# Optimization experiments

Measured on AMD Instinct MI355X. Metric: run time of the kernel, lower is better.

Reference implementation:

```python
import jax, jax.numpy as jnp
import numpy as np
from jax import lax

# Dims fixed by the module: Linear(96,24) => 16 channels * (24/4) length => per-step feature L=24
L = 24

def _conv1d(x, w, b):
    # x: (N, Cin, L), w: (Cout, Cin, K), 'same' padding for K=3
    y = lax.conv_general_dilated(x, w, window_strides=(1,), padding=[(1, 1)],
                                 dimension_numbers=("NCH", "OIH", "NCH"))
    return y + b[None, :, None]

def _maxpool2(x):
    # x: (N, C, L) -> (N, C, L//2), non-overlapping window of 2
    n, c, l = x.shape
    return x.reshape(n, c, l // 2, 2).max(axis=-1)

def setup_inputs() -> dict:
    key = jax.random.key(0)
    ks = jax.random.split(key, 11)
    S, B = 512, 256
    def u(k, shape, fan_in):
        bound = 1.0 / np.sqrt(fan_in)
        return jax.random.uniform(k, shape, jnp.float32, -bound, bound)
    return {
        "x":   jax.random.normal(ks[0], (S, B, L), jnp.float32),
        "w11": u(ks[1], (8, 1, 3), 1 * 3),   "b11": u(ks[2], (8,), 1 * 3),
        "w12": u(ks[3], (8, 8, 3), 8 * 3),   "b12": u(ks[4], (8,), 8 * 3),
        "w21": u(ks[5], (16, 8, 3), 8 * 3),  "b21": u(ks[6], (16,), 8 * 3),
        "w22": u(ks[7], (16, 16, 3), 16 * 3), "b22": u(ks[8], (16,), 16 * 3),
        "Wl":  u(ks[9], (24, 96), 96),        "bl": u(ks[10], (24,), 96),
    }

def reference(x, w11, b11, w12, b12, w21, b21, w22, b22, Wl, bl):
    # Original loops over timesteps applying the same CNN; timestep and batch
    # are independent, so fuse them into one conv batch (identical math).
    S, B, Lf = x.shape
    h = x.reshape(S * B, 1, Lf)                 # (SB, 1, 24)
    h = jax.nn.relu(_conv1d(h, w11, b11))       # (SB, 8, 24); Dropout(0.1) = identity in eval
    h = jax.nn.relu(_conv1d(h, w12, b12))       # (SB, 8, 24)
    h = _maxpool2(h)                            # (SB, 8, 12)
    h = jax.nn.relu(_conv1d(h, w21, b21))       # (SB, 16, 12); Dropout = identity in eval
    h = jax.nn.relu(_conv1d(h, w22, b22))       # (SB, 16, 12)
    h = _maxpool2(h)                            # (SB, 16, 6)
    h = h.reshape(S, B, 96)                     # torch reshape(batch, -1) per step
    return h @ Wl.T + bl                        # (S, B, 24)
```

## Files before the change

kernel.cpp:

```cpp
#include <hip/hip_runtime.h>


typedef _Float16 h2v __attribute__((ext_vector_type(2)));

__device__ __forceinline__ float fdot2(h2v a, h2v b, float c) {
    return __builtin_amdgcn_fdot2(a, b, c, false);
}
__device__ __forceinline__ unsigned packh2(float a, float b) {
    h2v p; p.x = (_Float16)a; p.y = (_Float16)b;
    return __builtin_bit_cast(unsigned, p);
}
__device__ __forceinline__ h2v ldh2(unsigned u) {
    return __builtin_bit_cast(h2v, u);
}

#define TPB 256

__launch_bounds__(TPB, 3)
__global__ void cnn_pre_lstm_kernel(
    const float* __restrict__ x,
    const float* __restrict__ w11, const float* __restrict__ b11,
    const float* __restrict__ w12, const float* __restrict__ b12,
    const float* __restrict__ w21, const float* __restrict__ b21,
    const float* __restrict__ w22, const float* __restrict__ b22,
    const float* __restrict__ Wl,  const float* __restrict__ bl,
    float* __restrict__ out)
{
    __shared__ unsigned sA_[6144];
    __shared__ unsigned sB_[3072];
    float* sInF  = (float*)sB_;
    float* sOutF = (float*)sA_;

    const int tid = threadIdx.x;
    const int ln  = tid & 63;
    const int wv  = __builtin_amdgcn_readfirstlane(tid >> 6);

    {
        const float* xg = x + (size_t)blockIdx.x * 1536;
        #pragma unroll
        for (int k = 0; k < 6; ++k) {
            int o = tid + k * TPB;
            int s = o / 24, p = o % 24;
            sInF[s * 25 + p] = xg[o];
        }
    }
    __syncthreads();

    {
        const int c0 = 2 * wv;
        const float wA0 = w11[c0*3+0], wA1 = w11[c0*3+1], wA2 = w11[c0*3+2];
        const float wB0 = w11[c0*3+3], wB1 = w11[c0*3+4], wB2 = w11[c0*3+5];
        const float bA = b11[c0], bB = b11[c0+1];

        float xv[24];
        #pragma unroll
        for (int p = 0; p < 24; ++p) xv[p] = sInF[ln*25 + p];

        #pragma unroll
        for (int p = 0; p < 24; ++p) {
            float a = bA, b = bB;
            if (p > 0)  { a = fmaf(wA0, xv[p-1], a); b = fmaf(wB0, xv[p-1], b); }
            a = fmaf(wA1, xv[p], a);  b = fmaf(wB1, xv[p], b);
            if (p < 23) { a = fmaf(wA2, xv[p+1], a); b = fmaf(wB2, xv[p+1], b); }
            sA_[wv*1536 + p*64 + ln] = packh2(fmaxf(a, 0.f), fmaxf(b, 0.f));
        }
    }
    __syncthreads();

    {
        const int c0 = 2 * wv;
        h2v wp[2][4][3];
        #pragma unroll
        for (int i = 0; i < 2; ++i)
            #pragma unroll
            for (int cp = 0; cp < 4; ++cp)
                #pragma unroll
                for (int k = 0; k < 3; ++k) {
                    const float* wr = w12 + (c0 + i) * 24;
                    wp[i][cp][k] = ldh2(packh2(wr[(2*cp)*3 + k], wr[(2*cp+1)*3 + k]));
                }
        float acc[2][24];
        {
            const float bb0 = b12[c0], bb1 = b12[c0+1];
            #pragma unroll
            for (int p = 0; p < 24; ++p) { acc[0][p] = bb0; acc[1][p] = bb1; }
        }
        #pragma unroll
        for (int cp = 0; cp < 4; ++cp) {
            h2v xv[24];
            #pragma unroll
            for (int p = 0; p < 24; ++p) xv[p] = ldh2(sA_[cp*1536 + p*64 + ln]);
            #pragma unroll
            for (int p = 0; p < 24; ++p) {
                #pragma unroll
                for (int i = 0; i < 2; ++i) {
                    if (p > 0)  acc[i][p] = fdot2(wp[i][cp][0], xv[p-1], acc[i][p]);
                    acc[i][p] = fdot2(wp[i][cp][1], xv[p], acc[i][p]);
                    if (p < 23) acc[i][p] = fdot2(wp[i][cp][2], xv[p+1], acc[i][p]);
                }
            }
        }
        #pragma unroll
        for (int q = 0; q < 12; ++q) {
            float r0 = fmaxf(fmaxf(acc[0][2*q], acc[0][2*q+1]), 0.f);
            float r1 = fmaxf(fmaxf(acc[1][2*q], acc[1][2*q+1]), 0.f);
            sB_[wv*768 + q*64 + ln] = packh2(r0, r1);
        }
    }
    __syncthreads();

    {
        const int c0 = 4 * wv;
        h2v wp[4][4][3];
        #pragma unroll
        for (int i = 0; i < 4; ++i)
            #pragma unroll
            for (int cp = 0; cp < 4; ++cp)
                #pragma unroll
                for (int k = 0; k < 3; ++k) {
                    const float* wr = w21 + (c0 + i) * 24;
                    wp[i][cp][k] = ldh2(packh2(wr[(2*cp)*3 + k], wr[(2*cp+1)*3 + k]));
                }
        float acc[4][12];
        #pragma unroll
        for (int i = 0; i < 4; ++i) {
            const float bb = b21[c0 + i];
            #pragma unroll
            for (int p = 0; p < 12; ++p) acc[i][p] = bb;
        }
        #pragma unroll
        for (int cp = 0; cp < 4; ++cp) {
            h2v xv[12];
            #pragma unroll
            for (int p = 0; p < 12; ++p) xv[p] = ldh2(sB_[cp*768 + p*64 + ln]);
            #pragma unroll
            for (int p = 0; p < 12; ++p) {
                #pragma unroll
                for (int i = 0; i < 4; ++i) {
                    if (p > 0)  acc[i][p] = fdot2(wp[i][cp][0], xv[p-1], acc[i][p]);
                    acc[i][p] = fdot2(wp[i][cp][1], xv[p], acc[i][p]);
                    if (p < 11) acc[i][p] = fdot2(wp[i][cp][2], xv[p+1], acc[i][p]);
                }
            }
        }
        #pragma unroll
        for (int pr = 0; pr < 2; ++pr)
            #pragma unroll
            for (int p = 0; p < 12; ++p)
                sA_[(2*wv + pr)*768 + p*64 + ln] =
                    packh2(fmaxf(acc[2*pr][p], 0.f), fmaxf(acc[2*pr+1][p], 0.f));
    }
    __syncthreads();

    {
        const int c0 = 4 * wv;
        float acc[4][12];
        #pragma unroll
        for (int i = 0; i < 4; ++i) {
            const float bb = b22[c0 + i];
            #pragma unroll
            for (int p = 0; p < 12; ++p) acc[i][p] = bb;
        }
        #pragma unroll
        for (int hh = 0; hh < 2; ++hh) {
            h2v wp[4][4][3];
            #pragma unroll
            for (int i = 0; i < 4; ++i)
                #pragma unroll
                for (int cp = 0; cp < 4; ++cp)
                    #pragma unroll
                    for (int k = 0; k < 3; ++k) {
                        const float* wr = w22 + (c0 + i) * 48;
                        const int ci0 = 2 * (4*hh + cp);
                        wp[i][cp][k] = ldh2(packh2(wr[ci0*3 + k], wr[(ci0+1)*3 + k]));
                    }
            #pragma unroll
            for (int cp = 0; cp < 4; ++cp) {
                const int gcp = 4*hh + cp;
                h2v xv[12];
                #pragma unroll
                for (int p = 0; p < 12; ++p) xv[p] = ldh2(sA_[gcp*768 + p*64 + ln]);
                #pragma unroll
                for (int p = 0; p < 12; ++p) {
                    #pragma unroll
                    for (int i = 0; i < 4; ++i) {
                        if (p > 0)  acc[i][p] = fdot2(wp[i][cp][0], xv[p-1], acc[i][p]);
                        acc[i][p] = fdot2(wp[i][cp][1], xv[p], acc[i][p]);
                        if (p < 11) acc[i][p] = fdot2(wp[i][cp][2], xv[p+1], acc[i][p]);
                    }
                }
            }
        }
        #pragma unroll
        for (int pr = 0; pr < 2; ++pr)
            #pragma unroll
            for (int q = 0; q < 6; ++q) {
                float r0 = fmaxf(fmaxf(acc[2*pr][2*q],   acc[2*pr][2*q+1]),   0.f);
                float r1 = fmaxf(fmaxf(acc[2*pr+1][2*q], acc[2*pr+1][2*q+1]), 0.f);
                sB_[(2*wv + pr)*384 + q*64 + ln] = packh2(r0, r1);
            }
    }
    __syncthreads();

    {
        const int j0 = 6 * wv;
        float v[96];
        #pragma unroll
        for (int cp = 0; cp < 8; ++cp)
            #pragma unroll
            for (int q = 0; q < 6; ++q) {
                h2v t = ldh2(sB_[cp*384 + q*64 + ln]);
                v[12*cp + q]     = (float)t.x;
                v[12*cp + q + 6] = (float)t.y;
            }
        float acc6[6];
        #pragma unroll
        for (int i = 0; i < 6; ++i) acc6[i] = bl[j0 + i];
        #pragma unroll
        for (int i = 0; i < 6; ++i) {
            const float4* wr = (const float4*)(Wl + (j0 + i) * 96);
            #pragma unroll
            for (int g = 0; g < 24; ++g) {
                float4 w4 = wr[g];
                acc6[i] = fmaf(w4.x, v[4*g+0], fmaf(w4.y, v[4*g+1],
                          fmaf(w4.z, v[4*g+2], fmaf(w4.w, v[4*g+3], acc6[i]))));
            }
        }
        #pragma unroll
        for (int i = 0; i < 6; ++i)
            sOutF[ln*25 + j0 + i] = acc6[i];
    }
    __syncthreads();

    {
        float* og = out + (size_t)blockIdx.x * 1536;
        #pragma unroll
        for (int k = 0; k < 6; ++k) {
            int o = tid + k * TPB;
            int s = o / 24, j = o % 24;
            og[o] = sOutF[s*25 + j];
        }
    }
}

extern "C" void kernel_launch(void* const* d_in, const int* in_sizes, int n_in,
                              void* d_out, int out_size, void* d_ws, size_t ws_size,
                              hipStream_t stream) {
    const float* x   = (const float*)d_in[0];
    const float* w11 = (const float*)d_in[1];
    const float* b11 = (const float*)d_in[2];
    const float* w12 = (const float*)d_in[3];
    const float* b12 = (const float*)d_in[4];
    const float* w21 = (const float*)d_in[5];
    const float* b21 = (const float*)d_in[6];
    const float* w22 = (const float*)d_in[7];
    const float* b22 = (const float*)d_in[8];
    const float* Wl  = (const float*)d_in[9];
    const float* bl  = (const float*)d_in[10];
    float* out = (float*)d_out;

    const int n_samples = in_sizes[0] / 24;
    const int blocks = n_samples / 64;

    hipLaunchKernelGGL(cnn_pre_lstm_kernel, dim3(blocks), dim3(TPB), 0, stream,
                       x, w11, b11, w12, b12, w21, b21, w22, b22, Wl, bl, out);
}
```

Measured before the change: 138.8 us.

## Prepack fp16 weights in a separate kernel, use fdot2 for linear, double block size

A small pre-kernel packs the conv and linear weights into fp16 pairs in workspace once per call, so the main kernel loads packed words instead of converting floats in every thread. The final linear layer now uses fp16 fdot2 on the packed activations and weights instead of fp32 FMAs. Blocks grow to 512 threads covering 128 samples, with twice the shared memory. The trade-offs are an extra kernel launch, lower precision in the linear layer, and possibly lower occupancy from the larger LDS footprint.

```diff
diff --git a/kernel.cpp b/kernel.cpp
--- a/kernel.cpp
+++ b/kernel.cpp
@@ -14,29 +14,60 @@
     return __builtin_bit_cast(h2v, u);
 }
 
-#define TPB 256
-
-__launch_bounds__(TPB, 3)
+#define W12P 0
+#define W21P 96
+#define W22P 288
+#define WLP  672
+#define NPACK 1824
+
+__global__ void pack_weights_kernel(
+    const float* __restrict__ w12, const float* __restrict__ w21,
+    const float* __restrict__ w22, const float* __restrict__ Wl,
+    unsigned* __restrict__ ws)
+{
+    for (int i = threadIdx.x; i < NPACK; i += 256) {
+        float a, b;
+        if (i < W21P) {
+            int t = i - W12P, co = t / 12, r = t % 12, cp = r / 3, k = r % 3;
+            a = w12[co*24 + (2*cp)*3 + k];  b = w12[co*24 + (2*cp+1)*3 + k];
+        } else if (i < W22P) {
+            int t = i - W21P, co = t / 12, r = t % 12, cp = r / 3, k = r % 3;
+            a = w21[co*24 + (2*cp)*3 + k];  b = w21[co*24 + (2*cp+1)*3 + k];
+        } else if (i < WLP) {
+            int t = i - W22P, co = t / 24, r = t % 24, cp = r / 3, k = r % 3;
+            a = w22[co*48 + (2*cp)*3 + k];  b = w22[co*48 + (2*cp+1)*3 + k];
+        } else {
+            int t = i - WLP, j = t / 48, r = t % 48, cp = r / 6, q = r % 6;
+            a = Wl[j*96 + 12*cp + q];       b = Wl[j*96 + 12*cp + q + 6];
+        }
+        ws[i] = packh2(a, b);
+    }
+}
+
+#define TPB 512
+
+__launch_bounds__(TPB, 4)
 __global__ void cnn_pre_lstm_kernel(
     const float* __restrict__ x,
     const float* __restrict__ w11, const float* __restrict__ b11,
-    const float* __restrict__ w12, const float* __restrict__ b12,
-    const float* __restrict__ w21, const float* __restrict__ b21,
-    const float* __restrict__ w22, const float* __restrict__ b22,
-    const float* __restrict__ Wl,  const float* __restrict__ bl,
+    const float* __restrict__ b12, const float* __restrict__ b21,
+    const float* __restrict__ b22, const float* __restrict__ bl,
+    const unsigned* __restrict__ wsp,
     float* __restrict__ out)
 {
-    __shared__ unsigned sA_[6144];
-    __shared__ unsigned sB_[3072];
+    __shared__ unsigned sA_[12288];
+    __shared__ unsigned sB_[6144];
     float* sInF  = (float*)sB_;
     float* sOutF = (float*)sA_;
 
     const int tid = threadIdx.x;
     const int ln  = tid & 63;
     const int wv  = __builtin_amdgcn_readfirstlane(tid >> 6);
-
-    {
-        const float* xg = x + (size_t)blockIdx.x * 1536;
+    const int cg  = wv & 3;
+    const int ls  = (wv >> 2) * 64 + ln;
+
+    {
+        const float* xg = x + (size_t)blockIdx.x * 3072;
         #pragma unroll
         for (int k = 0; k < 6; ++k) {
             int o = tid + k * TPB;
@@ -47,14 +78,14 @@
     __syncthreads();
 
     {
-        const int c0 = 2 * wv;
+        const int c0 = 2 * cg;
         const float wA0 = w11[c0*3+0], wA1 = w11[c0*3+1], wA2 = w11[c0*3+2];
         const float wB0 = w11[c0*3+3], wB1 = w11[c0*3+4], wB2 = w11[c0*3+5];
         const float bA = b11[c0], bB = b11[c0+1];
 
         float xv[24];
         #pragma unroll
-        for (int p = 0; p < 24; ++p) xv[p] = sInF[ln*25 + p];
+        for (int p = 0; p < 24; ++p) xv[p] = sInF[ls*25 + p];
 
         #pragma unroll
         for (int p = 0; p < 24; ++p) {
@@ -62,23 +93,21 @@
             if (p > 0)  { a = fmaf(wA0, xv[p-1], a); b = fmaf(wB0, xv[p-1], b); }
             a = fmaf(wA1, xv[p], a);  b = fmaf(wB1, xv[p], b);
             if (p < 23) { a = fmaf(wA2, xv[p+1], a); b = fmaf(wB2, xv[p+1], b); }
-            sA_[wv*1536 + p*64 + ln] = packh2(fmaxf(a, 0.f), fmaxf(b, 0.f));
-        }
-    }
-    __syncthreads();
-
-    {
-        const int c0 = 2 * wv;
+            sA_[cg*3072 + p*128 + ls] = packh2(fmaxf(a, 0.f), fmaxf(b, 0.f));
+        }
+    }
+    __syncthreads();
+
+    {
+        const int c0 = 2 * cg;
         h2v wp[2][4][3];
         #pragma unroll
         for (int i = 0; i < 2; ++i)
             #pragma unroll
             for (int cp = 0; cp < 4; ++cp)
                 #pragma unroll
-                for (int k = 0; k < 3; ++k) {
-                    const float* wr = w12 + (c0 + i) * 24;
-                    wp[i][cp][k] = ldh2(packh2(wr[(2*cp)*3 + k], wr[(2*cp+1)*3 + k]));
-                }
+                for (int k = 0; k < 3; ++k)
+                    wp[i][cp][k] = ldh2(wsp[W12P + (c0+i)*12 + cp*3 + k]);
         float acc[2][24];
         {
             const float bb0 = b12[c0], bb1 = b12[c0+1];
@@ -89,7 +118,7 @@
         for (int cp = 0; cp < 4; ++cp) {
             h2v xv[24];
             #pragma unroll
-            for (int p = 0; p < 24; ++p) xv[p] = ldh2(sA_[cp*1536 + p*64 + ln]);
+            for (int p = 0; p < 24; ++p) xv[p] = ldh2(sA_[cp*3072 + p*128 + ls]);
             #pragma unroll
             for (int p = 0; p < 24; ++p) {
                 #pragma unroll
@@ -104,23 +133,21 @@
         for (int q = 0; q < 12; ++q) {
             float r0 = fmaxf(fmaxf(acc[0][2*q], acc[0][2*q+1]), 0.f);
             float r1 = fmaxf(fmaxf(acc[1][2*q], acc[1][2*q+1]), 0.f);
-            sB_[wv*768 + q*64 + ln] = packh2(r0, r1);
-        }
-    }
-    __syncthreads();
-
-    {
-        const int c0 = 4 * wv;
+            sB_[cg*1536 + q*128 + ls] = packh2(r0, r1);
+        }
+    }
+    __syncthreads();
+
+    {
+        const int c0 = 4 * cg;
         h2v wp[4][4][3];
         #pragma unroll
         for (int i = 0; i < 4; ++i)
             #pragma unroll
             for (int cp = 0; cp < 4; ++cp)
                 #pragma unroll
-                for (int k = 0; k < 3; ++k) {
-                    const float* wr = w21 + (c0 + i) * 24;
-                    wp[i][cp][k] = ldh2(packh2(wr[(2*cp)*3 + k], wr[(2*cp+1)*3 + k]));
-                }
+                for (int k = 0; k < 3; ++k)
+                    wp[i][cp][k] = ldh2(wsp[W21P + (c0+i)*12 + cp*3 + k]);
         float acc[4][12];
         #pragma unroll
         for (int i = 0; i < 4; ++i) {
@@ -132,7 +159,7 @@
         for (int cp = 0; cp < 4; ++cp) {
             h2v xv[12];
             #pragma unroll
-            for (int p = 0; p < 12; ++p) xv[p] = ldh2(sB_[cp*768 + p*64 + ln]);
+            for (int p = 0; p < 12; ++p) xv[p] = ldh2(sB_[cp*1536 + p*128 + ls]);
             #pragma unroll
             for (int p = 0; p < 12; ++p) {
                 #pragma unroll
@@ -147,13 +174,13 @@
         for (int pr = 0; pr < 2; ++pr)
             #pragma unroll
             for (int p = 0; p < 12; ++p)
-                sA_[(2*wv + pr)*768 + p*64 + ln] =
+                sA_[(2*cg + pr)*1536 + p*128 + ls] =
                     packh2(fmaxf(acc[2*pr][p], 0.f), fmaxf(acc[2*pr+1][p], 0.f));
     }
     __syncthreads();
 
     {
-        const int c0 = 4 * wv;
+        const int c0 = 4 * cg;
         float acc[4][12];
         #pragma unroll
         for (int i = 0; i < 4; ++i) {
@@ -169,17 +196,14 @@
                 #pragma unroll
                 for (int cp = 0; cp < 4; ++cp)
                     #pragma unroll
-                    for (int k = 0; k < 3; ++k) {
-                        const float* wr = w22 + (c0 + i) * 48;
-                        const int ci0 = 2 * (4*hh + cp);
-                        wp[i][cp][k] = ldh2(packh2(wr[ci0*3 + k], wr[(ci0+1)*3 + k]));
-                    }
+                    for (int k = 0; k < 3; ++k)
+                        wp[i][cp][k] = ldh2(wsp[W22P + (c0+i)*24 + (4*hh+cp)*3 + k]);
             #pragma unroll
             for (int cp = 0; cp < 4; ++cp) {
                 const int gcp = 4*hh + cp;
                 h2v xv[12];
                 #pragma unroll
-                for (int p = 0; p < 12; ++p) xv[p] = ldh2(sA_[gcp*768 + p*64 + ln]);
+                for (int p = 0; p < 12; ++p) xv[p] = ldh2(sA_[gcp*1536 + p*128 + ls]);
                 #pragma unroll
                 for (int p = 0; p < 12; ++p) {
                     #pragma unroll
@@ -197,43 +221,43 @@
             for (int q = 0; q < 6; ++q) {
                 float r0 = fmaxf(fmaxf(acc[2*pr][2*q],   acc[2*pr][2*q+1]),   0.f);
                 float r1 = fmaxf(fmaxf(acc[2*pr+1][2*q], acc[2*pr+1][2*q+1]), 0.f);
-                sB_[(2*wv + pr)*384 + q*64 + ln] = packh2(r0, r1);
-            }
-    }
-    __syncthreads();
-
-    {
-        const int j0 = 6 * wv;
-        float v[96];
+                sB_[(2*cg + pr)*768 + q*128 + ls] = packh2(r0, r1);
+            }
+    }
+    __syncthreads();
+
+    {
+        const int j0 = 6 * cg;
+        h2v hv[8][6];
         #pragma unroll
         for (int cp = 0; cp < 8; ++cp)
             #pragma unroll
-            for (int q = 0; q < 6; ++q) {
-                h2v t = ldh2(sB_[cp*384 + q*64 + ln]);
-                v[12*cp + q]     = (float)t.x;
-                v[12*cp + q + 6] = (float)t.y;
-            }
+            for (int q = 0; q < 6; ++q)
+                hv[cp][q] = ldh2(sB_[cp*768 + q*128 + ls]);
+
         float acc6[6];
         #pragma unroll
         for (int i = 0; i < 6; ++i) acc6[i] = bl[j0 + i];
         #pragma unroll
         for (int i = 0; i < 6; ++i) {
-            const float4* wr = (const float4*)(Wl + (j0 + i) * 96);
-            #pragma unroll
-            for (int g = 0; g < 24; ++g) {
-                float4 w4 = wr[g];
-                acc6[i] = fmaf(w4.x, v[4*g+0], fmaf(w4.y, v[4*g+1],
-                          fmaf(w4.z, v[4*g+2], fmaf(w4.w, v[4*g+3], acc6[i]))));
+            #pragma unroll
+            for (int cp = 0; cp < 8; ++cp) {
+                #pragma unroll
+                for (int qq = 0; qq < 3; ++qq) {
+                    uint2 w2 = *(const uint2*)&wsp[WLP + (j0+i)*48 + cp*6 + 2*qq];
+                    acc6[i] = fdot2(ldh2(w2.x), hv[cp][2*qq],   acc6[i]);
+                    acc6[i] = fdot2(ldh2(w2.y), hv[cp][2*qq+1], acc6[i]);
+                }
             }
         }
         #pragma unroll
         for (int i = 0; i < 6; ++i)
-            sOutF[ln*25 + j0 + i] = acc6[i];
-    }
-    __syncthreads();
-
-    {
-        float* og = out + (size_t)blockIdx.x * 1536;
+            sOutF[ls*25 + j0 + i] = acc6[i];
+    }
+    __syncthreads();
+
+    {
+        float* og = out + (size_t)blockIdx.x * 3072;
         #pragma unroll
         for (int k = 0; k < 6; ++k) {
             int o = tid + k * TPB;
@@ -258,10 +282,14 @@
     const float* Wl  = (const float*)d_in[9];
     const float* bl  = (const float*)d_in[10];
     float* out = (float*)d_out;
+    unsigned* ws = (unsigned*)d_ws;
+
+    hipLaunchKernelGGL(pack_weights_kernel, dim3(1), dim3(256), 0, stream,
+                       w12, w21, w22, Wl, ws);
 
     const int n_samples = in_sizes[0] / 24;
-    const int blocks = n_samples / 64;
+    const int blocks = n_samples / 128;
 
     hipLaunchKernelGGL(cnn_pre_lstm_kernel, dim3(blocks), dim3(TPB), 0, stream,
-                       x, w11, b11, w12, b12, w21, b21, w22, b22, Wl, bl, out);
-}
+                       x, w11, b11, b12, b21, b22, bl, ws, out);
+}
```

Result: faster. 132.1 us (-4.8%).
